# Kernel optimization log

Hardware: AMD Instinct MI355X
Metric: run time of the kernel (lower is better)

## Reference

```python
import jax, jax.numpy as jnp
import numpy as np
from math import sqrt

N_HEADS = 16

def setup_inputs() -> dict:
    key = jax.random.key(0)
    ks = jax.random.split(key, 6)
    B, T, C = 4, 2048, 1024
    s = 0.02
    return {
        "X": jax.random.normal(ks[0], (B, T, C), jnp.float32),
        "Wq": jax.random.normal(ks[1], (C, C), jnp.float32) * s,
        "Wk": jax.random.normal(ks[2], (C, C), jnp.float32) * s,
        "Wv": jax.random.normal(ks[3], (C, C), jnp.float32) * s,
        "Wo": jax.random.normal(ks[4], (C, C), jnp.float32) * s,
        "bo": jnp.zeros((C,), jnp.float32),
    }

def reference(X, Wq, Wk, Wv, Wo, bo):
    B, T, C = X.shape
    H = N_HEADS
    D = C // H
    scale = sqrt(C / H)  # == sqrt(D)
    # Linear layers (torch Linear: y = x @ W.T), split into heads: [B,H,T,D]
    Q = (X @ Wq.T).reshape(B, T, H, D).transpose(0, 2, 1, 3)
    K = (X @ Wk.T).reshape(B, T, H, D).transpose(0, 2, 1, 3)
    V = (X @ Wv.T).reshape(B, T, H, D).transpose(0, 2, 1, 3)
    A = jnp.einsum("bhtd,bhsd->bhts", Q, K) / scale  # [B,H,T,T]
    causal = jnp.tril(jnp.ones((T, T), dtype=bool))
    A = jnp.where(causal, A, -jnp.inf)
    A = jax.nn.softmax(A, axis=-1)
    Y = jnp.einsum("bhts,bhsd->bhtd", A, V)  # [B,H,T,D]
    Y = Y.transpose(0, 2, 1, 3).reshape(B, T, C)
    return Y @ Wo.T + bo
```

## Files before the change

### kernel.cpp

```cpp
#include <hip/hip_runtime.h>
#include <hip/hip_bf16.h>
#include <stdint.h>


typedef unsigned short u16;
typedef __attribute__((ext_vector_type(8))) __bf16 bf16x8;
typedef __attribute__((ext_vector_type(4))) float  f32x4;
typedef __attribute__((ext_vector_type(4))) unsigned short u16x4;
typedef __attribute__((ext_vector_type(8))) unsigned short u16x8;
typedef __attribute__((ext_vector_type(4))) short s16x4;

#define B_  4
#define T_  2048
#define C_  1024
#define H_  16
#define D_  64
#define BT_ (B_ * T_)

#define Q_SCALE 0.1803368801111204f

__device__ __forceinline__ u16 f32_to_bf16(float f) {
    unsigned int u = __float_as_uint(f);
    unsigned int r = (u + 0x7FFFu + ((u >> 16) & 1u)) >> 16;
    return (u16)r;
}

__device__ __forceinline__ unsigned int pk_bf16(float a, float b) {
    float2 f2; f2.x = a; f2.y = b;
    __hip_bfloat162 h = __float22bfloat162_rn(f2);
    return *(unsigned int*)&h;
}

__device__ __forceinline__ void async16(const void* g, void* lds) {
    __builtin_amdgcn_global_load_lds(
        (const __attribute__((address_space(1))) void*)g,
        (__attribute__((address_space(3))) void*)lds, 16, 0, 0);
}

__global__ void cast_all_kernel(const float* __restrict__ X,
                                const float* __restrict__ w0, const float* __restrict__ w1,
                                const float* __restrict__ w2, const float* __restrict__ w3,
                                u16* __restrict__ xo,
                                u16* __restrict__ o0, u16* __restrict__ o1,
                                u16* __restrict__ o2, u16* __restrict__ o3) {
    int id = blockIdx.x;
    const float* in; u16* out; int i;
    if (id < 8192) {
        in = X; out = xo; i = id * 256 + threadIdx.x;
    } else {
        int k = (id - 8192) >> 10;
        in  = (k == 0) ? w0 : (k == 1) ? w1 : (k == 2) ? w2 : w3;
        out = (k == 0) ? o0 : (k == 1) ? o1 : (k == 2) ? o2 : o3;
        i = ((id - 8192) & 1023) * 256 + threadIdx.x;
    }
    float4 v = ((const float4*)in)[i];
    u16x4 o;
    o[0] = f32_to_bf16(v.x); o[1] = f32_to_bf16(v.y);
    o[2] = f32_to_bf16(v.z); o[3] = f32_to_bf16(v.w);
    ((u16x4*)out)[i] = o;
}

__global__ __launch_bounds__(256, 2) void qkv_gemm(
    const u16* __restrict__ Xb,
    const u16* __restrict__ Wqb, const u16* __restrict__ Wkb, const u16* __restrict__ Wvb,
    u16* __restrict__ Qb, u16* __restrict__ Kb, u16* __restrict__ Vtb)
{
    __shared__ u16 Xs[8192];
    __shared__ u16 Wqs[8192], Wks[8192], Wvs[8192];

    int id = blockIdx.x;
    int xcd = id & 7;
    int local = id >> 3;
    int tt = xcd * 8 + (local & 7);
    int ct = local >> 3;
    int m0 = tt * 128, n0 = ct * 128;

    int tid = threadIdx.x, lane = tid & 63, w = tid >> 6;
    int quad = lane >> 4, l15 = lane & 15;
    int wm = w >> 1, wn = w & 1;

    int c0 = tid, c1 = tid + 256;
    int row0 = c0 >> 2, row1 = c1 >> 2;
    int gc0 = (((c0 & 3) - (row0 >> 1)) & 3) * 8;
    int gc1 = (((c1 & 3) - (row1 >> 1)) & 3) * 8;
    int ldsb0 = (w * 64) * 16;
    int ldsb1 = (256 + w * 64) * 16;

    const u16* xp0 = Xb  + (size_t)(m0 + row0) * C_ + gc0;
    const u16* xp1 = Xb  + (size_t)(m0 + row1) * C_ + gc1;
    const u16* wq0 = Wqb + (size_t)(n0 + row0) * C_ + gc0;
    const u16* wq1 = Wqb + (size_t)(n0 + row1) * C_ + gc1;
    const u16* wk0 = Wkb + (size_t)(n0 + row0) * C_ + gc0;
    const u16* wk1 = Wkb + (size_t)(n0 + row1) * C_ + gc1;
    const u16* wv0 = Wvb + (size_t)(n0 + row0) * C_ + gc0;
    const u16* wv1 = Wvb + (size_t)(n0 + row1) * C_ + gc1;

    int aoff[4], boff[4];
#pragma unroll
    for (int i = 0; i < 4; ++i) {
        int rA = wm * 64 + i * 16 + l15;
        aoff[i] = (rA * 32 + (((rA >> 1) + quad) & 3) * 8) * 2;
        int rB = wn * 64 + i * 16 + l15;
        boff[i] = (rB * 32 + (((rB >> 1) + quad) & 3) * 8) * 2;
    }

    f32x4 aq[4][4], ak[4][4], av[4][4];
    const f32x4 z4 = {0.f, 0.f, 0.f, 0.f};
#pragma unroll
    for (int i = 0; i < 4; ++i)
#pragma unroll
        for (int j = 0; j < 4; ++j) { aq[i][j] = z4; ak[i][j] = z4; av[i][j] = z4; }

    async16(xp0, (char*)Xs  + ldsb0); async16(xp1, (char*)Xs  + ldsb1);
    async16(wq0, (char*)Wqs + ldsb0); async16(wq1, (char*)Wqs + ldsb1);
    async16(wk0, (char*)Wks + ldsb0); async16(wk1, (char*)Wks + ldsb1);
    async16(wv0, (char*)Wvs + ldsb0); async16(wv1, (char*)Wvs + ldsb1);
    xp0 += 32; xp1 += 32; wq0 += 32; wq1 += 32;
    wk0 += 32; wk1 += 32; wv0 += 32; wv1 += 32;

    auto body = [&](int kt, int cur, int nxt) {
        __syncthreads();
        if (kt + 1 < 32) {
            async16(xp0, (char*)Xs  + nxt + ldsb0); async16(xp1, (char*)Xs  + nxt + ldsb1);
            async16(wq0, (char*)Wqs + nxt + ldsb0); async16(wq1, (char*)Wqs + nxt + ldsb1);
            async16(wk0, (char*)Wks + nxt + ldsb0); async16(wk1, (char*)Wks + nxt + ldsb1);
            async16(wv0, (char*)Wvs + nxt + ldsb0); async16(wv1, (char*)Wvs + nxt + ldsb1);
        }
        xp0 += 32; xp1 += 32; wq0 += 32; wq1 += 32;
        wk0 += 32; wk1 += 32; wv0 += 32; wv1 += 32;

        bf16x8 xa[4];
#pragma unroll
        for (int i = 0; i < 4; ++i)
            xa[i] = *(const bf16x8*)((const char*)Xs + cur + aoff[i]);

        bf16x8 bb[4];
#pragma unroll
        for (int j = 0; j < 4; ++j)
            bb[j] = *(const bf16x8*)((const char*)Wqs + cur + boff[j]);
#pragma unroll
        for (int j = 0; j < 4; ++j)
#pragma unroll
            for (int i = 0; i < 4; ++i)
                aq[j][i] = __builtin_amdgcn_mfma_f32_16x16x32_bf16(bb[j], xa[i], aq[j][i], 0, 0, 0);

#pragma unroll
        for (int j = 0; j < 4; ++j)
            bb[j] = *(const bf16x8*)((const char*)Wks + cur + boff[j]);
#pragma unroll
        for (int j = 0; j < 4; ++j)
#pragma unroll
            for (int i = 0; i < 4; ++i)
                ak[j][i] = __builtin_amdgcn_mfma_f32_16x16x32_bf16(bb[j], xa[i], ak[j][i], 0, 0, 0);

#pragma unroll
        for (int j = 0; j < 4; ++j)
            bb[j] = *(const bf16x8*)((const char*)Wvs + cur + boff[j]);
#pragma unroll
        for (int i = 0; i < 4; ++i)
#pragma unroll
            for (int j = 0; j < 4; ++j)
                av[i][j] = __builtin_amdgcn_mfma_f32_16x16x32_bf16(xa[i], bb[j], av[i][j], 0, 0, 0);
    };

    for (int kt = 0; kt < 32; kt += 2) {
        body(kt,     0,    8192);
        body(kt + 1, 8192, 0);
    }

#pragma unroll
    for (int j = 0; j < 4; ++j) {
        int ch0 = n0 + wn * 64 + j * 16 + quad * 4;
#pragma unroll
        for (int i = 0; i < 4; ++i) {
            int t = m0 + wm * 64 + i * 16 + l15;
            u16x4 vq, vk;
#pragma unroll
            for (int r = 0; r < 4; ++r) {
                vq[r] = f32_to_bf16(aq[j][i][r] * Q_SCALE);
                vk[r] = f32_to_bf16(ak[j][i][r]);
            }
            *(u16x4*)&Qb[(size_t)t * C_ + ch0] = vq;
            *(u16x4*)&Kb[(size_t)t * C_ + ch0] = vk;
        }
    }
#pragma unroll
    for (int i = 0; i < 4; ++i) {
        int t0 = m0 + wm * 64 + i * 16 + quad * 4;
        int bb_ = t0 >> 11, tloc = t0 & (T_ - 1);
#pragma unroll
        for (int j = 0; j < 4; ++j) {
            int col = n0 + wn * 64 + j * 16 + l15;
            int h = col >> 6, d = col & 63;
            u16x4 v;
#pragma unroll
            for (int r = 0; r < 4; ++r) v[r] = f32_to_bf16(av[i][j][r]);
            *(u16x4*)&Vtb[(((bb_ * H_ + h) * D_ + d) * T_) + tloc] = v;
        }
    }
}

__device__ __forceinline__ void gemm_core_128_db(
    const u16* __restrict__ A, const u16* __restrict__ B,
    u16* As, u16* Bs, int m0, int n0, f32x4 (&acc)[4][4])
{
    const int K = C_;
    const int KT = K / 32;
    int tid  = threadIdx.x;
    int lane = tid & 63, w = tid >> 6;
    int quad = lane >> 4, l15 = lane & 15;
    int wm = w >> 1, wn = w & 1;

    int c0 = tid, c1 = tid + 256;
    int row0 = c0 >> 2, row1 = c1 >> 2;
    int gc0 = (((c0 & 3) - (row0 >> 1)) & 3) * 8;
    int gc1 = (((c1 & 3) - (row1 >> 1)) & 3) * 8;
    int ldsb0 = (w * 64) * 16;
    int ldsb1 = (256 + w * 64) * 16;

    const u16* ApA = A + (size_t)(m0 + row0) * K + gc0;
    const u16* ApB = A + (size_t)(m0 + row1) * K + gc1;
    const u16* BpA = B + (size_t)(n0 + row0) * K + gc0;
    const u16* BpB = B + (size_t)(n0 + row1) * K + gc1;

    char* As0 = (char*)As; char* As1 = (char*)As + 8192;
    char* Bs0 = (char*)Bs; char* Bs1 = (char*)Bs + 8192;

    int aoff[4], boff[4];
#pragma unroll
    for (int i = 0; i < 4; ++i) {
        int rA = wm * 64 + i * 16 + l15;
        aoff[i] = (rA * 32 + (((rA >> 1) + quad) & 3) * 8) * 2;
        int rB = wn * 64 + i * 16 + l15;
        boff[i] = (rB * 32 + (((rB >> 1) + quad) & 3) * 8) * 2;
    }

    async16(ApA, As0 + ldsb0); async16(ApB, As0 + ldsb1);
    async16(BpA, Bs0 + ldsb0); async16(BpB, Bs0 + ldsb1);
    ApA += 32; ApB += 32; BpA += 32; BpB += 32;

    auto body = [&](int kt, const char* Ac, const char* Bc, char* Apf, char* Bpf) {
        __syncthreads();
        if (kt + 1 < KT) {
            async16(ApA, Apf + ldsb0); async16(ApB, Apf + ldsb1);
            async16(BpA, Bpf + ldsb0); async16(BpB, Bpf + ldsb1);
        }
        ApA += 32; ApB += 32; BpA += 32; BpB += 32;

        bf16x8 a[4], b[4];
#pragma unroll
        for (int i = 0; i < 4; ++i) {
            a[i] = *(const bf16x8*)(Ac + aoff[i]);
            b[i] = *(const bf16x8*)(Bc + boff[i]);
        }
#pragma unroll
        for (int i = 0; i < 4; ++i)
#pragma unroll
            for (int j = 0; j < 4; ++j)
                acc[i][j] = __builtin_amdgcn_mfma_f32_16x16x32_bf16(a[i], b[j], acc[i][j], 0, 0, 0);
    };

    for (int kt = 0; kt < KT; kt += 2) {
        body(kt,     As0, Bs0, As1, Bs1);
        body(kt + 1, As1, Bs1, As0, Bs0);
    }
}

__global__ __launch_bounds__(256, 4) void attn_kernel(
    const u16* __restrict__ Qb, const u16* __restrict__ Kb,
    const u16* __restrict__ Vtb, u16* __restrict__ Yb)
{
    __shared__ u16 SMA[16384];
    u16* Ks0 = SMA;
    u16* Ks1 = SMA + 4096;
    u16* Vs0 = SMA + 8192;
    u16* Vs1 = SMA + 12288;

    int id = blockIdx.x;
    int bh = id & 63;
    int jj = id >> 6;

    int tid = threadIdx.x, lane = tid & 63, w = tid >> 6;
    int quad = lane >> 4, l15 = lane & 15;
    int b = bh >> 4, h = bh & 15;

    int koff0[4], koff1[4], voff[4][4];
#pragma unroll
    for (int sblk = 0; sblk < 4; ++sblk) {
        int sr = sblk * 16 + l15;
        koff0[sblk] = (sr * 64 + ((quad + sr) & 7) * 8) * 2;
        koff1[sblk] = (sr * 64 + ((4 + quad + sr) & 7) * 8) * 2;
    }
#pragma unroll
    for (int n = 0; n < 4; ++n)
#pragma unroll
        for (int sblk = 0; sblk < 4; ++sblk) {
            int dr = n * 16 + l15;
            voff[n][sblk] = (dr * 64 + ((sblk * 2 + (quad >> 1) + dr) & 7) * 8 + (quad & 1) * 4) * 2;
        }

    int cA = tid, cB = tid + 256;
    int sA = cA >> 3, sB = cB >> 3;
    int offA = (((cA & 7) - sA) & 7) * 8;
    int offB = (((cB & 7) - sB) & 7) * 8;
    const u16* Kbase = Kb + (size_t)(b * T_) * C_ + h * 64;
    const u16* Vbase = Vtb + (size_t)bh * D_ * T_;
    int ldsb0 = (w * 64) * 16, ldsb1 = (256 + w * 64) * 16;

    const s16x4 ones = { (short)0x3F80, (short)0x3F80, (short)0x3F80, (short)0x3F80 };
    const f32x4 z4 = {0.f, 0.f, 0.f, 0.f};

    int qts[2] = { jj, 31 - jj };

    for (int pass = 0; pass < 2; ++pass) {
        int qt = qts[pass];
        int qbase = qt * 64;

        if (pass) __syncthreads();

        bf16x8 qf0, qf1;
        {
            const u16* q0 = Qb + ((size_t)(b * T_ + qbase + w * 16 + l15)) * C_ + h * 64;
            qf0 = *(const bf16x8*)(q0 + quad * 8);
            qf1 = *(const bf16x8*)(q0 + 32 + quad * 8);
        }

        f32x4 o_acc[4];
        f32x4 l_acc = z4;
#pragma unroll
        for (int n = 0; n < 4; ++n) o_acc[n] = z4;

        const int nst = qt + 1;

        const u16* kgpA = Kbase + (size_t)sA * C_ + offA;
        const u16* kgpB = Kbase + (size_t)sB * C_ + offB;
        const u16* vgpA = Vbase + sA * T_ + offA;
        const u16* vgpB = Vbase + sB * T_ + offB;

        async16(kgpA, (char*)Ks0 + ldsb0);
        async16(kgpB, (char*)Ks0 + ldsb1);
        async16(vgpA, (char*)Vs0 + ldsb0);
        async16(vgpB, (char*)Vs0 + ldsb1);
        kgpA += 64 * C_; kgpB += 64 * C_; vgpA += 64; vgpB += 64;

        auto tile_body = [&](int st, const u16* K_, const u16* V_, char* Kpf, char* Vpf) {
            __syncthreads();
            if (st + 1 < nst) {
                async16(kgpA, Kpf + ldsb0);
                async16(kgpB, Kpf + ldsb1);
                async16(vgpA, Vpf + ldsb0);
                async16(vgpB, Vpf + ldsb1);
            }
            kgpA += 64 * C_; kgpB += 64 * C_; vgpA += 64; vgpB += 64;

            f32x4 sv[4];
#pragma unroll
            for (int sblk = 0; sblk < 4; ++sblk) {
                bf16x8 k0 = *(const bf16x8*)((const char*)K_ + koff0[sblk]);
                bf16x8 k1 = *(const bf16x8*)((const char*)K_ + koff1[sblk]);
                f32x4 t0 = __builtin_amdgcn_mfma_f32_16x16x32_bf16(k0, qf0, z4, 0, 0, 0);
                sv[sblk] = __builtin_amdgcn_mfma_f32_16x16x32_bf16(k1, qf1, t0, 0, 0, 0);
            }

            if (st == qt) {
                int tl = w * 16 + l15;
#pragma unroll
                for (int sblk = 0; sblk < 4; ++sblk)
#pragma unroll
                    for (int r = 0; r < 4; ++r)
                        if (sblk * 16 + quad * 4 + r > tl) sv[sblk][r] = -1e30f;
            }

            s16x4 pfrag[4];
#pragma unroll
            for (int sblk = 0; sblk < 4; ++sblk) {
#pragma unroll
                for (int r = 0; r < 4; ++r)
                    sv[sblk][r] = __builtin_amdgcn_exp2f(sv[sblk][r]);
                uint2 pk;
                pk.x = pk_bf16(sv[sblk][0], sv[sblk][1]);
                pk.y = pk_bf16(sv[sblk][2], sv[sblk][3]);
                pfrag[sblk] = *(s16x4*)&pk;
                l_acc = __builtin_amdgcn_mfma_f32_16x16x16bf16_1k(ones, pfrag[sblk], l_acc, 0, 0, 0);
            }

#pragma unroll
            for (int n = 0; n < 4; ++n)
#pragma unroll
                for (int sblk = 0; sblk < 4; ++sblk) {
                    s16x4 va = *(const s16x4*)((const char*)V_ + voff[n][sblk]);
                    o_acc[n] = __builtin_amdgcn_mfma_f32_16x16x16bf16_1k(va, pfrag[sblk], o_acc[n], 0, 0, 0);
                }
        };

        for (int st = 0; st < nst; st += 2) {
            tile_body(st, Ks0, Vs0, (char*)Ks1, (char*)Vs1);
            if (st + 1 < nst)
                tile_body(st + 1, Ks1, Vs1, (char*)Ks0, (char*)Vs0);
        }

        __syncthreads();
        u16* PW = SMA + w * 1152;
        {
            float inv = 1.0f / l_acc[0];
#pragma unroll
            for (int n = 0; n < 4; ++n) {
                uint2 pk;
                pk.x = pk_bf16(o_acc[n][0] * inv, o_acc[n][1] * inv);
                pk.y = pk_bf16(o_acc[n][2] * inv, o_acc[n][3] * inv);
                *(u16x4*)&PW[l15 * 72 + n * 16 + quad * 4] = *(u16x4*)&pk;
            }
        }
        asm volatile("s_waitcnt lgkmcnt(0)" ::: "memory");
#pragma unroll
        for (int st = 0; st < 2; ++st) {
            int tr = st * 8 + (lane >> 3);
            int d8 = (lane & 7) * 8;
            u16x8 v = *(u16x8*)&PW[tr * 72 + d8];
            *(u16x8*)&Yb[(size_t)(b * T_ + qbase + w * 16 + tr) * C_ + h * 64 + d8] = v;
        }
    }
}

__global__ __launch_bounds__(256, 4) void proj_gemm(
    const u16* __restrict__ Yb, const u16* __restrict__ Wob,
    const float* __restrict__ bo, float* __restrict__ out)
{
    __shared__ u16 SM[17408];
    u16* As = SM;
    u16* Bs = SM + 8192;

    int id = blockIdx.x;
    int xcd = id & 7;
    int local = id >> 3;
    int by = xcd * 8 + (local & 7);
    int bx = local >> 3;
    int m0 = bx * 128, n0 = by * 128;

    f32x4 acc[4][4];
    const f32x4 z4 = {0.f, 0.f, 0.f, 0.f};
#pragma unroll
    for (int i = 0; i < 4; ++i)
#pragma unroll
        for (int j = 0; j < 4; ++j) acc[i][j] = z4;

    gemm_core_128_db(Wob, Yb, As, Bs, m0, n0, acc);

    int lane = threadIdx.x & 63, w = threadIdx.x >> 6;
    int quad = lane >> 4, l15 = lane & 15;
    int wm = w >> 1, wn = w & 1;

    float* LF = (float*)SM;
    __syncthreads();
#pragma unroll
    for (int hh = 0; hh < 2; ++hh) {
        if (wm == hh) {
#pragma unroll
            for (int i = 0; i < 4; ++i) {
                int chl = i * 16 + quad * 4;
#pragma unroll
                for (int j = 0; j < 4; ++j) {
                    int tl = wn * 64 + j * 16 + l15;
                    *(f32x4*)&LF[tl * 68 + chl] = acc[i][j];
                }
            }
        }
        __syncthreads();
        f32x4 b4 = *(const f32x4*)&bo[m0 + hh * 64 + (lane & 15) * 4];
#pragma unroll
        for (int st = 0; st < 8; ++st) {
            int tl = w * 32 + st * 4 + (lane >> 4);
            int ch4 = (lane & 15) * 4;
            f32x4 v = *(f32x4*)&LF[tl * 68 + ch4];
            v += b4;
            *(f32x4*)&out[(size_t)(n0 + tl) * C_ + m0 + hh * 64 + ch4] = v;
        }
        if (hh == 0) __syncthreads();
    }
}

extern "C" void kernel_launch(void* const* d_in, const int* in_sizes, int n_in,
                              void* d_out, int out_size, void* d_ws, size_t ws_size,
                              hipStream_t stream) {
    const float* X  = (const float*)d_in[0];
    const float* Wq = (const float*)d_in[1];
    const float* Wk = (const float*)d_in[2];
    const float* Wv = (const float*)d_in[3];
    const float* Wo = (const float*)d_in[4];
    const float* bo = (const float*)d_in[5];

    char* ws = (char*)d_ws;
    u16* Xb  = (u16*)(ws);
    u16* Wqb = (u16*)(ws + (16u << 20));
    u16* Wkb = (u16*)(ws + (18u << 20));
    u16* Wvb = (u16*)(ws + (20u << 20));
    u16* Wob = (u16*)(ws + (22u << 20));
    u16* Qb  = (u16*)(ws + (24u << 20));
    u16* Kb  = (u16*)(ws + (40u << 20));
    u16* Vtb = (u16*)(ws + (56u << 20));
    u16* Yb  = (u16*)(ws + (72u << 20));

    cast_all_kernel<<<dim3(8192 + 4 * 1024), 256, 0, stream>>>(
        X, Wq, Wk, Wv, Wo, Xb, Wqb, Wkb, Wvb, Wob);

    qkv_gemm<<<dim3(512), 256, 0, stream>>>(Xb, Wqb, Wkb, Wvb, Qb, Kb, Vtb);
    attn_kernel<<<dim3(1024), 256, 0, stream>>>(Qb, Kb, Vtb, Yb);
    proj_gemm<<<dim3(8 * 64), 256, 0, stream>>>(Yb, Wob, bo, (float*)d_out);
}
```

Measured before the change: 256.6 us.

## Rewrite QKV and output projection GEMMs as 8-wave 128x256 pipelined tiles

Replaces the QKV and projection GEMMs with a shared 512-thread core that computes 128x256 tiles. It uses a deeper async global-to-LDS pipeline with explicit vmcnt waits, raw barriers and setprio around the MFMA blocks. The QKV kernel no longer computes all three matrices per block; it spreads Q, K and V tiles across 768 blocks with XCD-aware mapping. The projection epilogue now writes directly from registers instead of staging through LDS. This aims to hide load latency and improve MFMA utilisation, at the cost of 96KB of LDS per block and less-coalesced direct stores.

Result: faster. 242.2 us (-5.6%).

```diff
diff --git a/kernel.cpp b/kernel.cpp
--- a/kernel.cpp
+++ b/kernel.cpp
@@ -16,6 +16,7 @@
 #define H_  16
 #define D_  64
 #define BT_ (B_ * T_)
+#define NT_ 16
 
 #define Q_SCALE 0.1803368801111204f
 
@@ -60,209 +61,152 @@
     ((u16x4*)out)[i] = o;
 }
 
-__global__ __launch_bounds__(256, 2) void qkv_gemm(
+template<bool SWAP>
+__device__ __forceinline__ void gemm8_core(const u16* __restrict__ Arow,
+                                           const u16* __restrict__ Brow,
+                                           char* lds, f32x4 (&acc)[4][4])
+{
+    int tid  = threadIdx.x;
+    int lane = tid & 63, w = tid >> 6;
+    int quad = lane >> 4, l15 = lane & 15;
+    int wm = w >> 2, wn = w & 3;
+
+    int r  = tid >> 2, s4 = tid & 3;
+    int kg = ((s4 - (r >> 1)) & 3) * 8;
+    const u16* xsrc  = Arow + (size_t)r * C_ + kg;
+    const u16* wsrc0 = Brow + (size_t)r * C_ + kg;
+    const u16* wsrc1 = Brow + (size_t)(128 + r) * C_ + kg;
+    int wu = w << 10;
+
+    int xoff[4], woff[4];
+#pragma unroll
+    for (int i = 0; i < 4; ++i) {
+        int rx = wm * 64 + i * 16 + l15;
+        xoff[i] = rx * 64 + (((rx >> 1) + quad) & 3) * 16;
+        int rw = wn * 64 + i * 16 + l15;
+        woff[i] = 16384 + rw * 64 + (((rw >> 1) + quad) & 3) * 16;
+    }
+
+    auto issue_group = [&](int g) {
+        int db = (g >> 1) & 1, ks = g & 1;
+        int koff = (g >> 1) * 64 + ks * 32;
+        char* ldb = lds + db * 49152;
+        async16(xsrc  + koff, ldb + ks * 8192 + wu);
+        async16(wsrc0 + koff, ldb + 16384 + ks * 16384 + wu);
+        async16(wsrc1 + koff, ldb + 16384 + ks * 16384 + 8192 + wu);
+    };
+
+    issue_group(0); issue_group(1); issue_group(2);
+    asm volatile("s_waitcnt vmcnt(6)" ::: "memory");
+    __builtin_amdgcn_s_barrier();
+    asm volatile("" ::: "memory");
+
+    for (int t = 0; t < NT_; ++t) {
+        char* cb = lds + (t & 1) * 49152;
+#pragma unroll
+        for (int p = 0; p < 2; ++p) {
+            bf16x8 xf[4], wf[4];
+            const char* xb = cb + p * 8192;
+            const char* wb = cb + p * 16384;
+#pragma unroll
+            for (int i = 0; i < 4; ++i) xf[i] = *(const bf16x8*)(xb + xoff[i]);
+#pragma unroll
+            for (int j = 0; j < 4; ++j) wf[j] = *(const bf16x8*)(wb + woff[j]);
+
+            int g = 2 * t + 3 + p;
+            if (g < 2 * NT_) issue_group(g);
+
+            if (t < NT_ - 2) {
+                asm volatile("s_waitcnt vmcnt(6)" ::: "memory");
+            } else if (t == NT_ - 2) {
+                if (p == 0) asm volatile("s_waitcnt vmcnt(6)" ::: "memory");
+                else        asm volatile("s_waitcnt vmcnt(3)" ::: "memory");
+            } else {
+                if (p == 0) asm volatile("s_waitcnt vmcnt(0)" ::: "memory");
+            }
+            asm volatile("" ::: "memory");
+            __builtin_amdgcn_s_barrier();
+            asm volatile("" ::: "memory");
+
+            __builtin_amdgcn_s_setprio(1);
+#pragma unroll
+            for (int i = 0; i < 4; ++i)
+#pragma unroll
+                for (int j = 0; j < 4; ++j) {
+                    if (SWAP)
+                        acc[i][j] = __builtin_amdgcn_mfma_f32_16x16x32_bf16(xf[i], wf[j], acc[i][j], 0, 0, 0);
+                    else
+                        acc[i][j] = __builtin_amdgcn_mfma_f32_16x16x32_bf16(wf[j], xf[i], acc[i][j], 0, 0, 0);
+                }
+            __builtin_amdgcn_s_setprio(0);
+            asm volatile("" ::: "memory");
+            __builtin_amdgcn_s_barrier();
+            asm volatile("" ::: "memory");
+        }
+    }
+}
+
+__global__ __launch_bounds__(512, 2) void qkv_gemm8(
     const u16* __restrict__ Xb,
     const u16* __restrict__ Wqb, const u16* __restrict__ Wkb, const u16* __restrict__ Wvb,
     u16* __restrict__ Qb, u16* __restrict__ Kb, u16* __restrict__ Vtb)
 {
-    __shared__ u16 Xs[8192];
-    __shared__ u16 Wqs[8192], Wks[8192], Wvs[8192];
+    __shared__ __attribute__((aligned(128))) char LDSRAW[98304];
 
     int id = blockIdx.x;
-    int xcd = id & 7;
-    int local = id >> 3;
-    int tt = xcd * 8 + (local & 7);
-    int ct = local >> 3;
-    int m0 = tt * 128, n0 = ct * 128;
+    int wg = (id & 7) * 96 + (id >> 3);
+    int bm = wg / 12, bn = wg % 12;
+    int m0 = bm * 128;
+    int nmat = bn >> 2;
+    int chb  = (bn & 3) * 256;
+
+    const u16* Wsel = (nmat == 0) ? Wqb : (nmat == 1) ? Wkb : Wvb;
+    const u16* Arow = Xb   + (size_t)m0  * C_;
+    const u16* Brow = Wsel + (size_t)chb * C_;
+
+    f32x4 acc[4][4];
+    const f32x4 z4 = {0.f, 0.f, 0.f, 0.f};
+#pragma unroll
+    for (int i = 0; i < 4; ++i)
+#pragma unroll
+        for (int j = 0; j < 4; ++j) acc[i][j] = z4;
 
     int tid = threadIdx.x, lane = tid & 63, w = tid >> 6;
     int quad = lane >> 4, l15 = lane & 15;
-    int wm = w >> 1, wn = w & 1;
-
-    int c0 = tid, c1 = tid + 256;
-    int row0 = c0 >> 2, row1 = c1 >> 2;
-    int gc0 = (((c0 & 3) - (row0 >> 1)) & 3) * 8;
-    int gc1 = (((c1 & 3) - (row1 >> 1)) & 3) * 8;
-    int ldsb0 = (w * 64) * 16;
-    int ldsb1 = (256 + w * 64) * 16;
-
-    const u16* xp0 = Xb  + (size_t)(m0 + row0) * C_ + gc0;
-    const u16* xp1 = Xb  + (size_t)(m0 + row1) * C_ + gc1;
-    const u16* wq0 = Wqb + (size_t)(n0 + row0) * C_ + gc0;
-    const u16* wq1 = Wqb + (size_t)(n0 + row1) * C_ + gc1;
-    const u16* wk0 = Wkb + (size_t)(n0 + row0) * C_ + gc0;
-    const u16* wk1 = Wkb + (size_t)(n0 + row1) * C_ + gc1;
-    const u16* wv0 = Wvb + (size_t)(n0 + row0) * C_ + gc0;
-    const u16* wv1 = Wvb + (size_t)(n0 + row1) * C_ + gc1;
-
-    int aoff[4], boff[4];
-#pragma unroll
-    for (int i = 0; i < 4; ++i) {
-        int rA = wm * 64 + i * 16 + l15;
-        aoff[i] = (rA * 32 + (((rA >> 1) + quad) & 3) * 8) * 2;
-        int rB = wn * 64 + i * 16 + l15;
-        boff[i] = (rB * 32 + (((rB >> 1) + quad) & 3) * 8) * 2;
-    }
-
-    f32x4 aq[4][4], ak[4][4], av[4][4];
-    const f32x4 z4 = {0.f, 0.f, 0.f, 0.f};
-#pragma unroll
-    for (int i = 0; i < 4; ++i)
-#pragma unroll
-        for (int j = 0; j < 4; ++j) { aq[i][j] = z4; ak[i][j] = z4; av[i][j] = z4; }
-
-    async16(xp0, (char*)Xs  + ldsb0); async16(xp1, (char*)Xs  + ldsb1);
-    async16(wq0, (char*)Wqs + ldsb0); async16(wq1, (char*)Wqs + ldsb1);
-    async16(wk0, (char*)Wks + ldsb0); async16(wk1, (char*)Wks + ldsb1);
-    async16(wv0, (char*)Wvs + ldsb0); async16(wv1, (char*)Wvs + ldsb1);
-    xp0 += 32; xp1 += 32; wq0 += 32; wq1 += 32;
-    wk0 += 32; wk1 += 32; wv0 += 32; wv1 += 32;
-
-    auto body = [&](int kt, int cur, int nxt) {
-        __syncthreads();
-        if (kt + 1 < 32) {
-            async16(xp0, (char*)Xs  + nxt + ldsb0); async16(xp1, (char*)Xs  + nxt + ldsb1);
-            async16(wq0, (char*)Wqs + nxt + ldsb0); async16(wq1, (char*)Wqs + nxt + ldsb1);
-            async16(wk0, (char*)Wks + nxt + ldsb0); async16(wk1, (char*)Wks + nxt + ldsb1);
-            async16(wv0, (char*)Wvs + nxt + ldsb0); async16(wv1, (char*)Wvs + nxt + ldsb1);
-        }
-        xp0 += 32; xp1 += 32; wq0 += 32; wq1 += 32;
-        wk0 += 32; wk1 += 32; wv0 += 32; wv1 += 32;
-
-        bf16x8 xa[4];
-#pragma unroll
-        for (int i = 0; i < 4; ++i)
-            xa[i] = *(const bf16x8*)((const char*)Xs + cur + aoff[i]);
-
-        bf16x8 bb[4];
-#pragma unroll
-        for (int j = 0; j < 4; ++j)
-            bb[j] = *(const bf16x8*)((const char*)Wqs + cur + boff[j]);
-#pragma unroll
-        for (int j = 0; j < 4; ++j)
-#pragma unroll
-            for (int i = 0; i < 4; ++i)
-                aq[j][i] = __builtin_amdgcn_mfma_f32_16x16x32_bf16(bb[j], xa[i], aq[j][i], 0, 0, 0);
-
-#pragma unroll
-        for (int j = 0; j < 4; ++j)
-            bb[j] = *(const bf16x8*)((const char*)Wks + cur + boff[j]);
-#pragma unroll
-        for (int j = 0; j < 4; ++j)
-#pragma unroll
-            for (int i = 0; i < 4; ++i)
-                ak[j][i] = __builtin_amdgcn_mfma_f32_16x16x32_bf16(bb[j], xa[i], ak[j][i], 0, 0, 0);
-
-#pragma unroll
-        for (int j = 0; j < 4; ++j)
-            bb[j] = *(const bf16x8*)((const char*)Wvs + cur + boff[j]);
-#pragma unroll
-        for (int i = 0; i < 4; ++i)
-#pragma unroll
-            for (int j = 0; j < 4; ++j)
-                av[i][j] = __builtin_amdgcn_mfma_f32_16x16x32_bf16(xa[i], bb[j], av[i][j], 0, 0, 0);
-    };
-
-    for (int kt = 0; kt < 32; kt += 2) {
-        body(kt,     0,    8192);
-        body(kt + 1, 8192, 0);
-    }
-
-#pragma unroll
-    for (int j = 0; j < 4; ++j) {
-        int ch0 = n0 + wn * 64 + j * 16 + quad * 4;
+    int wm = w >> 2, wn = w & 3;
+
+    if (nmat < 2) {
+        gemm8_core<false>(Arow, Brow, LDSRAW, acc);
+        u16* OUT = nmat ? Kb : Qb;
+        float scale = nmat ? 1.0f : Q_SCALE;
 #pragma unroll
         for (int i = 0; i < 4; ++i) {
-            int t = m0 + wm * 64 + i * 16 + l15;
-            u16x4 vq, vk;
-#pragma unroll
-            for (int r = 0; r < 4; ++r) {
-                vq[r] = f32_to_bf16(aq[j][i][r] * Q_SCALE);
-                vk[r] = f32_to_bf16(ak[j][i][r]);
-            }
-            *(u16x4*)&Qb[(size_t)t * C_ + ch0] = vq;
-            *(u16x4*)&Kb[(size_t)t * C_ + ch0] = vk;
-        }
-    }
-#pragma unroll
-    for (int i = 0; i < 4; ++i) {
-        int t0 = m0 + wm * 64 + i * 16 + quad * 4;
-        int bb_ = t0 >> 11, tloc = t0 & (T_ - 1);
-#pragma unroll
-        for (int j = 0; j < 4; ++j) {
-            int col = n0 + wn * 64 + j * 16 + l15;
-            int h = col >> 6, d = col & 63;
-            u16x4 v;
-#pragma unroll
-            for (int r = 0; r < 4; ++r) v[r] = f32_to_bf16(av[i][j][r]);
-            *(u16x4*)&Vtb[(((bb_ * H_ + h) * D_ + d) * T_) + tloc] = v;
-        }
-    }
-}
-
-__device__ __forceinline__ void gemm_core_128_db(
-    const u16* __restrict__ A, const u16* __restrict__ B,
-    u16* As, u16* Bs, int m0, int n0, f32x4 (&acc)[4][4])
-{
-    const int K = C_;
-    const int KT = K / 32;
-    int tid  = threadIdx.x;
-    int lane = tid & 63, w = tid >> 6;
-    int quad = lane >> 4, l15 = lane & 15;
-    int wm = w >> 1, wn = w & 1;
-
-    int c0 = tid, c1 = tid + 256;
-    int row0 = c0 >> 2, row1 = c1 >> 2;
-    int gc0 = (((c0 & 3) - (row0 >> 1)) & 3) * 8;
-    int gc1 = (((c1 & 3) - (row1 >> 1)) & 3) * 8;
-    int ldsb0 = (w * 64) * 16;
-    int ldsb1 = (256 + w * 64) * 16;
-
-    const u16* ApA = A + (size_t)(m0 + row0) * K + gc0;
-    const u16* ApB = A + (size_t)(m0 + row1) * K + gc1;
-    const u16* BpA = B + (size_t)(n0 + row0) * K + gc0;
-    const u16* BpB = B + (size_t)(n0 + row1) * K + gc1;
-
-    char* As0 = (char*)As; char* As1 = (char*)As + 8192;
-    char* Bs0 = (char*)Bs; char* Bs1 = (char*)Bs + 8192;
-
-    int aoff[4], boff[4];
-#pragma unroll
-    for (int i = 0; i < 4; ++i) {
-        int rA = wm * 64 + i * 16 + l15;
-        aoff[i] = (rA * 32 + (((rA >> 1) + quad) & 3) * 8) * 2;
-        int rB = wn * 64 + i * 16 + l15;
-        boff[i] = (rB * 32 + (((rB >> 1) + quad) & 3) * 8) * 2;
-    }
-
-    async16(ApA, As0 + ldsb0); async16(ApB, As0 + ldsb1);
-    async16(BpA, Bs0 + ldsb0); async16(BpB, Bs0 + ldsb1);
-    ApA += 32; ApB += 32; BpA += 32; BpB += 32;
-
-    auto body = [&](int kt, const char* Ac, const char* Bc, char* Apf, char* Bpf) {
-        __syncthreads();
-        if (kt + 1 < KT) {
-            async16(ApA, Apf + ldsb0); async16(ApB, Apf + ldsb1);
-            async16(BpA, Bpf + ldsb0); async16(BpB, Bpf + ldsb1);
-        }
-        ApA += 32; ApB += 32; BpA += 32; BpB += 32;
-
-        bf16x8 a[4], b[4];
+            size_t trow = (size_t)(m0 + wm * 64 + i * 16 + l15) * C_;
+#pragma unroll
+            for (int j = 0; j < 4; ++j) {
+                int ch = chb + wn * 64 + j * 16 + quad * 4;
+                u16x4 v;
+#pragma unroll
+                for (int rr = 0; rr < 4; ++rr) v[rr] = f32_to_bf16(acc[i][j][rr] * scale);
+                *(u16x4*)&OUT[trow + ch] = v;
+            }
+        }
+    } else {
+        gemm8_core<true>(Arow, Brow, LDSRAW, acc);
 #pragma unroll
         for (int i = 0; i < 4; ++i) {
-            a[i] = *(const bf16x8*)(Ac + aoff[i]);
-            b[i] = *(const bf16x8*)(Bc + boff[i]);
-        }
-#pragma unroll
-        for (int i = 0; i < 4; ++i)
-#pragma unroll
-            for (int j = 0; j < 4; ++j)
-                acc[i][j] = __builtin_amdgcn_mfma_f32_16x16x32_bf16(a[i], b[j], acc[i][j], 0, 0, 0);
-    };
-
-    for (int kt = 0; kt < KT; kt += 2) {
-        body(kt,     As0, Bs0, As1, Bs1);
-        body(kt + 1, As1, Bs1, As0, Bs0);
+            int t0 = m0 + wm * 64 + i * 16 + quad * 4;
+            int bb_ = t0 >> 11, tloc = t0 & (T_ - 1);
+#pragma unroll
+            for (int j = 0; j < 4; ++j) {
+                int ch = chb + wn * 64 + j * 16 + l15;
+                int h = ch >> 6, d = ch & 63;
+                u16x4 v;
+#pragma unroll
+                for (int rr = 0; rr < 4; ++rr) v[rr] = f32_to_bf16(acc[i][j][rr]);
+                *(u16x4*)&Vtb[(size_t)((bb_ * H_ + h) * D_ + d) * T_ + tloc] = v;
+            }
+        }
     }
 }
 
@@ -422,20 +366,16 @@
     }
 }
 
-__global__ __launch_bounds__(256, 4) void proj_gemm(
+__global__ __launch_bounds__(512, 2) void proj_gemm8(
     const u16* __restrict__ Yb, const u16* __restrict__ Wob,
     const float* __restrict__ bo, float* __restrict__ out)
 {
-    __shared__ u16 SM[17408];
-    u16* As = SM;
-    u16* Bs = SM + 8192;
+    __shared__ __attribute__((aligned(128))) char LDSRAW[98304];
 
     int id = blockIdx.x;
-    int xcd = id & 7;
-    int local = id >> 3;
-    int by = xcd * 8 + (local & 7);
-    int bx = local >> 3;
-    int m0 = bx * 128, n0 = by * 128;
+    int wg = (id & 7) * 32 + (id >> 3);
+    int bm = wg >> 2, bn = wg & 3;
+    int m0 = bm * 128, n0 = bn * 256;
 
     f32x4 acc[4][4];
     const f32x4 z4 = {0.f, 0.f, 0.f, 0.f};
@@ -444,38 +384,22 @@
 #pragma unroll
         for (int j = 0; j < 4; ++j) acc[i][j] = z4;
 
-    gemm_core_128_db(Wob, Yb, As, Bs, m0, n0, acc);
-
-    int lane = threadIdx.x & 63, w = threadIdx.x >> 6;
+    gemm8_core<false>(Yb + (size_t)m0 * C_, Wob + (size_t)n0 * C_, LDSRAW, acc);
+
+    int tid = threadIdx.x, lane = tid & 63, w = tid >> 6;
     int quad = lane >> 4, l15 = lane & 15;
-    int wm = w >> 1, wn = w & 1;
-
-    float* LF = (float*)SM;
-    __syncthreads();
-#pragma unroll
-    for (int hh = 0; hh < 2; ++hh) {
-        if (wm == hh) {
-#pragma unroll
-            for (int i = 0; i < 4; ++i) {
-                int chl = i * 16 + quad * 4;
-#pragma unroll
-                for (int j = 0; j < 4; ++j) {
-                    int tl = wn * 64 + j * 16 + l15;
-                    *(f32x4*)&LF[tl * 68 + chl] = acc[i][j];
-                }
-            }
-        }
-        __syncthreads();
-        f32x4 b4 = *(const f32x4*)&bo[m0 + hh * 64 + (lane & 15) * 4];
-#pragma unroll
-        for (int st = 0; st < 8; ++st) {
-            int tl = w * 32 + st * 4 + (lane >> 4);
-            int ch4 = (lane & 15) * 4;
-            f32x4 v = *(f32x4*)&LF[tl * 68 + ch4];
-            v += b4;
-            *(f32x4*)&out[(size_t)(n0 + tl) * C_ + m0 + hh * 64 + ch4] = v;
-        }
-        if (hh == 0) __syncthreads();
+    int wm = w >> 2, wn = w & 3;
+
+#pragma unroll
+    for (int j = 0; j < 4; ++j) {
+        int ch = n0 + wn * 64 + j * 16 + quad * 4;
+        f32x4 bv = *(const f32x4*)&bo[ch];
+#pragma unroll
+        for (int i = 0; i < 4; ++i) {
+            int t = m0 + wm * 64 + i * 16 + l15;
+            f32x4 v = acc[i][j] + bv;
+            *(f32x4*)&out[(size_t)t * C_ + ch] = v;
+        }
     }
 }
 
@@ -503,7 +427,7 @@
     cast_all_kernel<<<dim3(8192 + 4 * 1024), 256, 0, stream>>>(
         X, Wq, Wk, Wv, Wo, Xb, Wqb, Wkb, Wvb, Wob);
 
-    qkv_gemm<<<dim3(512), 256, 0, stream>>>(Xb, Wqb, Wkb, Wvb, Qb, Kb, Vtb);
+    qkv_gemm8<<<dim3(768), 512, 0, stream>>>(Xb, Wqb, Wkb, Wvb, Qb, Kb, Vtb);
     attn_kernel<<<dim3(1024), 256, 0, stream>>>(Qb, Kb, Vtb, Yb);
-    proj_gemm<<<dim3(8 * 64), 256, 0, stream>>>(Yb, Wob, bo, (float*)d_out);
-}
+    proj_gemm8<<<dim3(256), 512, 0, stream>>>(Yb, Wob, bo, (float*)d_out);
+}
```
